# Kernel optimization log

Hardware: AMD Instinct MI355X
Metric: run time of the kernel (lower is better)

## Reference

```python
import jax, jax.numpy as jnp
import numpy as np
import math

NHEADS = 4


def _mab(Q, K, qw, qb, kw, kb, vw, vb, ow, ob, mask):
    """MAB2 from tripletformer: multi-head attention (head split via cat(split,0)),
    softmax scale uses sqrt(FULL dim_V), masked_fill(mask==0, -1e10), residual on
    the projected Q, then O + relu(fc_o(O))."""
    dv = qw.shape[1]
    dh = dv // NHEADS
    B, Nq, _ = Q.shape
    Nk = K.shape[1]
    Qh = (Q @ qw + qb).reshape(B, Nq, NHEADS, dh).transpose(0, 2, 1, 3)  # B,h,Nq,dh
    Kh = (K @ kw + kb).reshape(B, Nk, NHEADS, dh).transpose(0, 2, 1, 3)
    Vh = (K @ vw + vb).reshape(B, Nk, NHEADS, dh).transpose(0, 2, 1, 3)
    att = jnp.einsum('bhqd,bhkd->bhqk', Qh, Kh) * (1.0 / math.sqrt(dv))
    att = jnp.where(mask, att, jnp.asarray(-1e10, att.dtype))
    A = jax.nn.softmax(att, axis=-1)
    Oh = Qh + jnp.einsum('bhqk,bhkd->bhqd', A, Vh)
    O = Oh.transpose(0, 2, 1, 3).reshape(B, Nq, dv)
    return O + jax.nn.relu(O @ ow + ob)


def _forward(context_x, value, mask, obs_len, iff_w, iff_b, ind_points,
             q0w, q0b, k0w, k0b, v0w, v0b, o0w, o0b,
             q1w, q1b, k1w, k1b, v1w, v1b, o1w, o1b):
    B, L = context_x.shape
    D = value.shape[-1]
    mflat = mask.reshape(B, L * D)
    # stable stream compaction: observed entries first, original (time-major,
    # channel-minor) order preserved; truncate to static obs_len
    order = jnp.argsort(-mflat, axis=-1, stable=True)[:, :obs_len]  # (B, N)
    T = jnp.broadcast_to(context_x[:, :, None], (B, L, D)).reshape(B, L * D)
    C = jnp.broadcast_to(jnp.arange(D, dtype=jnp.int32), (B, L, D)).reshape(B, L * D)
    U = value.reshape(B, L * D)
    take = lambda a: jnp.take_along_axis(a, order, axis=-1)
    T_, U_, mk_ = take(T), take(U), take(mflat)
    Ch = jax.nn.one_hot(take(C), D, dtype=value.dtype)  # one_hot(num_classes=dim-2)
    X = jnp.concatenate([Ch, T_[..., None], U_[..., None]], axis=-1) * mk_[..., None]
    Y = jax.nn.relu(X @ iff_w + iff_b) * mk_[..., None]
    key_valid = mk_ > 0                        # (B, N)
    mask1 = key_valid[:, None, None, :]        # mab0: mask padded keys
    mask2 = key_valid[:, None, :, None]        # mab1: mask padded query rows
    Z = Y
    n_layers = ind_points.shape[0]
    for i in range(n_layers):
        I = jnp.broadcast_to(ind_points[i], (B,) + ind_points[i].shape)
        H = _mab(I, Z, q0w[i], q0b[i], k0w[i], k0b[i], v0w[i], v0b[i], o0w[i], o0b[i], mask1)
        Zn = _mab(Z, H, q1w[i], q1b[i], k1w[i], k1b[i], v1w[i], v1b[i], o1w[i], o1b[i], mask2)
        Z = Zn * mk_[..., None] + Z
    return Z, mk_[..., None]


def setup_inputs() -> dict:
    B, L, D, OBS, DK, M, NL = 16, 512, 41, 4096, 128, 128, 3
    key = jax.random.key(0)
    ks = jax.random.split(key, 16)
    context_x = jnp.sort(jax.random.uniform(ks[0], (B, L), dtype=jnp.float32), axis=-1)
    value = jax.random.normal(ks[1], (B, L, D), dtype=jnp.float32)
    # exactly OBS observed entries per batch row -> static packed length
    r = jax.random.uniform(ks[2], (B, L * D))
    kth = jnp.sort(r, axis=-1)[:, OBS]
    mask = (r < kth[:, None]).astype(jnp.float32).reshape(B, L, D)

    def w(k, shape, fan):
        return jax.random.normal(k, shape, dtype=jnp.float32) / math.sqrt(fan)

    inp = dict(
        context_x=context_x, value=value, mask=mask, obs_len=OBS,
        iff_w=w(ks[3], (D + 2, DK), D + 2), iff_b=jnp.zeros((DK,), jnp.float32),
        ind_points=w(ks[4], (NL, M, DK), DK),
    )
    for j, n in enumerate(['q0', 'k0', 'v0', 'o0', 'q1', 'k1', 'v1', 'o1']):
        inp[n + 'w'] = w(ks[5 + j], (NL, DK, DK), DK)
        inp[n + 'b'] = jnp.zeros((NL, DK), jnp.float32)
    return inp


def reference(context_x, value, mask, obs_len, iff_w, iff_b, ind_points,
              q0w, q0b, k0w, k0b, v0w, v0b, o0w, o0b,
              q1w, q1b, k1w, k1b, v1w, v1b, o1w, o1b):
    return _forward(context_x, value, mask, obs_len, iff_w, iff_b, ind_points,
                    q0w, q0b, k0w, k0b, v0w, v0b, o0w, o0b,
                    q1w, q1b, k1w, k1b, v1w, v1b, o1w, o1b)
```

## Files before the change

kernel.cpp:

```cpp
#include <hip/hip_runtime.h>
#include <math.h>

#define NBATCH 16
#define SEQL   512
#define DIM    41
#define LDFLAT (SEQL*DIM)
#define OBS    4096
#define DK     128
#define NH     4
#define DH     32

typedef short bf16x8 __attribute__((ext_vector_type(8)));
typedef short short8v __attribute__((ext_vector_type(8)));
typedef float floatx4 __attribute__((ext_vector_type(4)));

__device__ __forceinline__ short f2bf(float f) {
  union { float f; unsigned u; } v;
  v.f = f;
  unsigned r = (v.u + 0x7fffu + ((v.u >> 16) & 1u)) >> 16;
  return (short)r;
}
__device__ __forceinline__ float bf2f(short s) {
  union { unsigned u; float f; } v;
  v.u = ((unsigned)(unsigned short)s) << 16;
// ... 18 lines not shown
#pragma unroll
  for (int k = 0; k < 4; k++) {
    int i = tid * 8 + k * 2048;
    *(int4*)&Wl[swz(i >> 7, i & 127)] = s.v[k];
  }
}
typedef struct { int4 v[2]; } WStageF;
__device__ __forceinline__ void stage_load_f(WStageF& s,
                                             const short* __restrict__ W,
                                             int tid) {
#pragma unroll
  for (int k = 0; k < 2; k++)
    s.v[k] = *(const int4*)&W[(size_t)tid * 8 + (size_t)k * 8192];
}
__device__ __forceinline__ void stage_write_f(short* Wl, const WStageF& s,
                                              int tid) {
#pragma unroll
  for (int k = 0; k < 2; k++) {
    int i = tid * 8 + k * 8192;
    *(int4*)&Wl[swz(i >> 7, i & 127)] = s.v[k];
  }
}

__device__ __forceinline__ void gemm4_s(const short* Wl, const bf16x8 af[4],
                                        int lm, int quad, floatx4 acc[4]) {
#pragma unroll
  for (int nt = 0; nt < 4; nt++) acc[nt] = (floatx4){0.f, 0.f, 0.f, 0.f};
#pragma unroll
  for (int kc = 0; kc < 4; kc++) {
    bf16x8 a = af[kc];
#pragma unroll
    for (int nt = 0; nt < 4; nt++) {
      bf16x8 b = *(const bf16x8*)&Wl[swz(nt * 16 + lm, kc * 32 + quad * 8)];
      acc[nt] = __builtin_amdgcn_mfma_f32_16x16x32_bf16(a, b, acc[nt], 0, 0, 0);
    }
  }
}
__device__ __forceinline__ void gemm2_s(const short* Wl, const bf16x8 af[4],
                                        int colq, int lm, int quad,
                                        floatx4 acc[2]) {
#pragma unroll
  for (int nt = 0; nt < 2; nt++) acc[nt] = (floatx4){0.f, 0.f, 0.f, 0.f};
#pragma unroll
  for (int kc = 0; kc < 4; kc++) {
    bf16x8 a = af[kc];
#pragma unroll
    for (int nt = 0; nt < 2; nt++) {
      bf16x8 b = *(const bf16x8*)&Wl[swz(colq * 32 + nt * 16 + lm,
                                         kc * 32 + quad * 8)];
      acc[nt] = __builtin_amdgcn_mfma_f32_16x16x32_bf16(a, b, acc[nt], 0, 0, 0);
    }
  }
}
__device__ __forceinline__ void load_af_s(const short* Xl, int strip, int lm,
                                          int quad, bf16x8 af[4]) {
#pragma unroll
  for (int kc = 0; kc < 4; kc++)
    af[kc] = *(const bf16x8*)&Xl[swz(strip * 16 + lm, kc * 32 + quad * 8)];
}
__device__ __forceinline__ void store_sl4(short* Sl, const floatx4 acc[4],
                                          const float* __restrict__ bias,
                                          int wv, int lm, int quad,
                                          int colbase) {
#pragma unroll
  for (int nt = 0; nt < 4; nt++) {
    int col = colbase + nt * 16 + lm;
    float bn = bias[col];
#pragma unroll
    for (int r = 0; r < 4; r++)
      Sl[swz(wv * 16 + quad * 4 + r, col)] = f2bf(acc[nt][r] + bn);
  }
}
__device__ __forceinline__ void write_hs_s(const short* Sl,
                                           short* __restrict__ out, int rb,
                                           int nshift, int tid) {
  int rr = tid >> 2, hh = tid & 3;
  int r = rb + rr;
  int bb = r >> nshift, nn = r & ((1 << nshift) - 1);
  size_t o = (((size_t)(bb * NH + hh) << nshift) + nn) * 32;
#pragma unroll
  for (int j = 0; j < 4; j++)
    *(int4*)&out[o + j * 8] = *(int4*)&Sl[swz(rr, hh * 32 + j * 8)];
}
__device__ __forceinline__ void write_hs_q(const short* Sl,
                                           short* __restrict__ out, int rb,
                                           int nshift, int strip, int colq,
                                           int lane) {
  int rr = strip * 16 + (lane >> 2);
  int r = rb + rr;
  int bb = r >> nshift, nn = r & ((1 << nshift) - 1);
  size_t o = (((size_t)(bb * NH + colq) << nshift) + nn) * 32 + (lane & 3) * 8;
  *(int4*)&out[o] = *(const int4*)&Sl[swz(rr, colq * 32 + (lane & 3) * 8)];
}

__global__ __launch_bounds__(1024) void prep_build_kernel(
    const float* __restrict__ q0w, const float* __restrict__ k0w,
    const float* __restrict__ v0w, const float* __restrict__ o0w,
    const float* __restrict__ q1w, const float* __restrict__ k1w,
    const float* __restrict__ v1w, const float* __restrict__ o1w,
    short* __restrict__ Wt,
    const float* __restrict__ mask, int* __restrict__ order,
    float* __restrict__ mk_out, float* __restrict__ mk_out2) {
  __shared__ float Tl[128 * 132];
  __shared__ int wsums[16];
  __shared__ int s_total_ones;
  __shared__ int s_chunk_ones;
  __shared__ int s_ones_base;
  __shared__ int s_zeros_base;
  int tid = threadIdx.x;

  if (blockIdx.x < 24) {
    int id = blockIdx.x, l = id >> 3, wi = id & 7;
    const float* s;
    switch (wi) {
      case 0: s = q0w; break; case 1: s = k0w; break;
      case 2: s = v0w; break; case 3: s = o0w; break;
      case 4: s = q1w; break; case 5: s = k1w; break;
      case 6: s = v1w; break; default: s = o1w; break;
    }
    s += (size_t)l * 16384;
    for (int i = tid * 4; i < 16384; i += 4096) {
      int k = i >> 7, n = i & 127;
      float4 x = *(const float4*)&s[i];
      Tl[k * 132 + n + 0] = x.x; Tl[k * 132 + n + 1] = x.y;
      Tl[k * 132 + n + 2] = x.z; Tl[k * 132 + n + 3] = x.w;
    }
    __syncthreads();
    short* dst = Wt + (size_t)id * 16384;
    int n = tid >> 3, k0 = (tid & 7) * 16;
    for (int jc = 0; jc < 2; jc++) {
      short8v t;
#pragma unroll
      for (int j = 0; j < 8; j++) t[j] = f2bf(Tl[(k0 + jc * 8 + j) * 132 + n]);
      *(short8v*)&dst[n * 128 + k0 + jc * 8] = t;
    }
// ... 8 lines not shown
  for (int j = tid; j < LDFLAT; j += 1024) cnt += (m[j] > 0.f) ? 1 : 0;
  for (int off = 32; off > 0; off >>= 1) cnt += __shfl_xor(cnt, off);
  if (lane == 0) wsums[w] = cnt;
  __syncthreads();
  if (tid == 0) {
    int t = 0;
    for (int i = 0; i < 16; i++) t += wsums[i];
    s_total_ones = t; s_ones_base = 0; s_zeros_base = 0;
  }
  __syncthreads();
  int total_ones = s_total_ones;

  for (int c0 = 0; c0 < LDFLAT; c0 += 1024) {
    __syncthreads();
    int j = c0 + tid;
    bool valid = (j < LDFLAT);
    float mv = valid ? m[j] : 0.f;
    int one = (valid && mv > 0.f) ? 1 : 0;
    int v = one;
    for (int off = 1; off < 64; off <<= 1) {
      int t = __shfl_up(v, (unsigned)off);
      if (lane >= off) v += t;
    }
    if (lane == 63) wsums[w] = v;
    __syncthreads();
    if (tid == 0) {
      int run = 0;
      for (int i = 0; i < 16; i++) { int t = wsums[i]; wsums[i] = run; run += t; }
      s_chunk_ones = run;
    }
    __syncthreads();
    int ones_before = (v - one) + wsums[w];
    int ob = s_ones_base, zb = s_zeros_base, chunk_ones = s_chunk_ones;
    int rem = LDFLAT - c0;
    int chunk_valid = rem < 1024 ? rem : 1024;
    int valid_before = tid < rem ? tid : rem;
    if (valid) {
      int pos = one ? (ob + ones_before)
                    : (total_ones + zb + (valid_before - ones_before));
      if (pos < OBS) {
        order[b * OBS + pos] = j;
        mk_out[b * OBS + pos] = mv;
        mk_out2[b * OBS + pos] = mv;
      }
    }
    __syncthreads();
    if (tid == 0) {
      s_ones_base = ob + chunk_ones;
      s_zeros_base = zb + (chunk_valid - chunk_ones);
    }
  }
}

__global__ __launch_bounds__(256, 3) void fusedA_kernel(
    const int* __restrict__ order, const float* __restrict__ mk_g,
    const float* __restrict__ cx, const float* __restrict__ value,
    const float* __restrict__ iff_w, const float* __restrict__ iff_b,
    float* __restrict__ Z,
    const short* __restrict__ Wk, const float* __restrict__ kbias,
    short* __restrict__ Kb,
    const short* __restrict__ Wv, const float* __restrict__ vbias,
    short* __restrict__ Vb,
    const short* __restrict__ Wq, const float* __restrict__ qbias,
    short* __restrict__ Qb,
    const float* __restrict__ indp, const short* __restrict__ WtAll,
    const float* __restrict__ q0b_all, short* __restrict__ qh_b) {
  __shared__ __align__(16) short Xl[64 * 128];
  __shared__ __align__(16) short WlA[64 * 128];
  __shared__ __align__(16) short WlB[64 * 128];
  int tid = threadIdx.x;
  int wv = tid >> 6, lane = tid & 63, lm = lane & 15, quad = lane >> 4;
  int r_l = lane >> 2, seg = lane & 3;
  int lrow = wv * 16 + r_l;

  if (blockIdx.x >= 1024) {
    int id = blockIdx.x - 1024;
    int l = id >> 1, rbq = (id & 1) * 64;
    const float* X = indp + (size_t)l * 16384 + (size_t)rbq * 128;
    const short* W = WtAll + (size_t)(l * 8) * 16384;
    const float* bias = q0b_all + (size_t)l * 128;
    short* out = qh_b + (size_t)l * 16384;
    WStageH sA, sB;
    stage_load_h(sA, W, tid);
    stage_load_h(sB, W + 8192, tid);
    const float* Xr = X + (size_t)lrow * 128;
#pragma unroll
    for (int jj = 0; jj < 8; jj++) {
      int col = seg * 32 + jj * 4;
      float4 x = *(const float4*)&Xr[col];
      *(short4*)&Xl[swz(lrow, col)] =
          make_short4(f2bf(x.x), f2bf(x.y), f2bf(x.z), f2bf(x.w));
    }
    stage_write_h(WlA, sA, tid);
    stage_write_h(WlB, sB, tid);
    __syncthreads();
    bf16x8 af[4];
    load_af_s(Xl, wv, lm, quad, af);
    floatx4 acc[4];
    gemm4_s(WlA, af, lm, quad, acc);
    store_sl4(Xl, acc, bias, wv, lm, quad, 0);
    gemm4_s(WlB, af, lm, quad, acc);
    store_sl4(Xl, acc, bias, wv, lm, quad, 64);
    write_hs_s(Xl, out, rbq, 7, tid);
    return;
  }

  int rb = blockIdx.x * 64;
  WStageH s0; stage_load_h(s0, Wk, tid);
  int grow = rb + lrow;
  int bb = grow >> 12;
  int j = order[grow];
  int l = j / DIM, d = j - l * DIM;
  float t = cx[bb * SEQL + l];
  float u = value[(size_t)bb * LDFLAT + j];
  float mkv = mk_g[grow];
#pragma unroll
  for (int jj = 0; jj < 8; jj++) {
    int col = seg * 32 + jj * 4;
    float4 w0 = *(const float4*)&iff_w[d * DK + col];
    float4 w1 = *(const float4*)&iff_w[41 * DK + col];
    float4 w2 = *(const float4*)&iff_w[42 * DK + col];
    float4 b4 = *(const float4*)&iff_b[col];
    float4 z;
    z.x = fmaxf(w0.x + t * w1.x + u * w2.x + b4.x, 0.f) * mkv;
    z.y = fmaxf(w0.y + t * w1.y + u * w2.y + b4.y, 0.f) * mkv;
    z.z = fmaxf(w0.z + t * w1.z + u * w2.z + b4.z, 0.f) * mkv;
    z.w = fmaxf(w0.w + t * w1.w + u * w2.w + b4.w, 0.f) * mkv;
    *(float4*)&Z[(size_t)grow * DK + col] = z;
    *(short4*)&Xl[swz(lrow, col)] =
        make_short4(f2bf(z.x), f2bf(z.y), f2bf(z.z), f2bf(z.w));
  }
  stage_write_h(WlA, s0, tid);
  __syncthreads();
  WStageH s1; stage_load_h(s1, Wk + 8192, tid);
  bf16x8 af[4];
  load_af_s(Xl, wv, lm, quad, af);
  floatx4 acc[4];
  gemm4_s(WlA, af, lm, quad, acc);
  store_sl4(Xl, acc, kbias, wv, lm, quad, 0);
  stage_write_h(WlB, s1, tid);
  __syncthreads();
  WStageH s2; stage_load_h(s2, Wv, tid);
  gemm4_s(WlB, af, lm, quad, acc);
  store_sl4(Xl, acc, kbias, wv, lm, quad, 64);
  write_hs_s(Xl, Kb, rb, 12, tid);
  stage_write_h(WlA, s2, tid);
  __syncthreads();
  WStageH s3; stage_load_h(s3, Wv + 8192, tid);
  gemm4_s(WlA, af, lm, quad, acc);
  store_sl4(Xl, acc, vbias, wv, lm, quad, 0);
  stage_write_h(WlB, s3, tid);
  __syncthreads();
  WStageH s4; stage_load_h(s4, Wq, tid);
  gemm4_s(WlB, af, lm, quad, acc);
  store_sl4(Xl, acc, vbias, wv, lm, quad, 64);
  write_hs_s(Xl, Vb, rb, 12, tid);
  stage_write_h(WlA, s4, tid);
  __syncthreads();
  WStageH s5; stage_load_h(s5, Wq + 8192, tid);
  gemm4_s(WlA, af, lm, quad, acc);
  store_sl4(Xl, acc, qbias, wv, lm, quad, 0);
  stage_write_h(WlB, s5, tid);
  __syncthreads();
  gemm4_s(WlB, af, lm, quad, acc);
  store_sl4(Xl, acc, qbias, wv, lm, quad, 64);
  write_hs_s(Xl, Qb, rb, 12, tid);
}

__global__ __launch_bounds__(256) void attn1_kernel(
    const short* __restrict__ Qh,
    const short* __restrict__ Kh, const short* __restrict__ Vh,
    const float* __restrict__ mk,
    float* __restrict__ Opart, float* __restrict__ mpart,
    float* __restrict__ lpart) {
  __shared__ __align__(16) short Ql[128 * 40];
  __shared__ __align__(16) short Kc[64 * 40];
  __shared__ __align__(16) short Vtc[32 * 72];
  __shared__ __align__(16) short Pl[128 * 72];
  __shared__ float mkc[64];
  int bh = blockIdx.x;
  int b = bh >> 2, h = bh & 3;
  int ks = blockIdx.y;
  int tid = threadIdx.x;
  int wv = tid >> 6, lane = tid & 63, lm = lane & 15, quad = lane >> 4;

  const short* qbg = Qh + (size_t)h * 128 * 32;
  for (int i = tid * 8; i < 128 * 32; i += 2048) {
    int r = i >> 5, c = i & 31;
    *(int4*)&Ql[r * 40 + c] = *(const int4*)&qbg[i];
  }
  __syncthreads();
  bf16x8 aq[2];
  aq[0] = *(bf16x8*)&Ql[(wv * 32 + lm) * 40 + quad * 8];
  aq[1] = *(bf16x8*)&Ql[(wv * 32 + 16 + lm) * 40 + quad * 8];

  float m_i[2][4], l_i[2][4];
  floatx4 oacc[2][2];
#pragma unroll
  for (int mt = 0; mt < 2; mt++) {
#pragma unroll
    for (int r = 0; r < 4; r++) { m_i[mt][r] = -1e30f; l_i[mt][r] = 0.f; }
    oacc[mt][0] = (floatx4){0.f, 0.f, 0.f, 0.f};
    oacc[mt][1] = (floatx4){0.f, 0.f, 0.f, 0.f};
  }
  const float scale = 0.08838834764831845f;
  const short* kbase = Kh + ((size_t)bh * OBS + ks * 512) * 32;
  const short* vbase = Vh + ((size_t)bh * OBS + ks * 512) * 32;
  const float* mkb = mk + (size_t)b * OBS + ks * 512;

  for (int ch = 0; ch < 8; ch++) {
    __syncthreads();
    {
      int i = tid * 8;
      int r = i >> 5, c = i & 31;
      *(int4*)&Kc[r * 40 + c] = *(const int4*)&kbase[ch * 2048 + i];
      int4 vv4 = *(const int4*)&vbase[ch * 2048 + i];
      short* vv = (short*)&vv4;
#pragma unroll
      for (int j = 0; j < 8; j++) Vtc[(c + j) * 72 + r] = vv[j];
// ... 132 lines not shown
    o4.z = f2bf(bf2f(qs[2]) + oa2 * li);
    o4.w = f2bf(bf2f(qs[3]) + oa3 * li);
    *(short4*)&Xl[swz(rr, hh * 32 + c4)] = o4;
  }
  stage_write_f(WlA, sWo, tid);
  __syncthreads();
  bf16x8 afO[4];
  load_af_s(Xl, strip, lm, quad, afO);
  __syncthreads();
  WStageF sWk; stage_load_f(sWk, Wk, tid);
  floatx4 acc[2];
  gemm2_s(WlA, afO, colq, lm, quad, acc);
#pragma unroll
  for (int nt = 0; nt < 2; nt++) {
    int col = colq * 32 + nt * 16 + lm;
    float bn = obias[col];
#pragma unroll
    for (int r = 0; r < 4; r++) {
      int row = strip * 16 + quad * 4 + r;
      float ov = bf2f(Xl[swz(row, col)]);
      Xl[swz(row, col)] = f2bf(ov + fmaxf(acc[nt][r] + bn, 0.f));
    }
  }
  stage_write_f(WlB, sWk, tid);
  __syncthreads();
  bf16x8 afH[4];
  load_af_s(Xl, strip, lm, quad, afH);
  __syncthreads();
  WStageF sWv; stage_load_f(sWv, Wv, tid);
  gemm2_s(WlB, afH, colq, lm, quad, acc);
#pragma unroll
  for (int nt = 0; nt < 2; nt++) {
    int col = colq * 32 + nt * 16 + lm;
    float bn = kbias[col];
#pragma unroll
    for (int r = 0; r < 4; r++)
      Xl[swz(strip * 16 + quad * 4 + r, col)] = f2bf(acc[nt][r] + bn);
  }
  write_hs_q(Xl, khb, rb, 7, strip, colq, lane);
  stage_write_f(WlA, sWv, tid);
  __syncthreads();
  gemm2_s(WlA, afH, colq, lm, quad, acc);
#pragma unroll
  for (int nt = 0; nt < 2; nt++) {
    int col = colq * 32 + nt * 16 + lm;
    float bn = vbias[col];
#pragma unroll
    for (int r = 0; r < 4; r++)
      Xl[swz(strip * 16 + quad * 4 + r, col)] = f2bf(acc[nt][r] + bn);
  }
  write_hs_q(Xl, vhb, rb, 7, strip, colq, lane);
}

__global__ __launch_bounds__(256) void attn2_kernel(
    const short* __restrict__ Qh, const short* __restrict__ Kh,
    const short* __restrict__ Vh, short* __restrict__ O) {
  __shared__ __align__(16) short Kl[128 * 40];
  __shared__ __align__(16) short Vt[32 * 136];
  __shared__ __align__(16) short Ql[64 * 40];
  __shared__ __align__(16) short Pl[64 * 136];
  int bh = blockIdx.x;
  int b = bh >> 2, h = bh & 3;
  int q0 = blockIdx.y * 64;
  int tid = threadIdx.x;
  int wv = tid >> 6, lane = tid & 63, lm = lane & 15, quad = lane >> 4;
  const short* kb = Kh + (size_t)bh * 128 * 32;
  const short* vb = Vh + (size_t)bh * 128 * 32;
  const short* qb = Qh + ((size_t)bh * OBS + q0) * 32;

  for (int i = tid * 8; i < 128 * 32; i += 2048) {
    int r = i >> 5, c = i & 31;
    *(int4*)&Kl[r * 40 + c] = *(const int4*)&kb[i];
  }
  for (int i = tid * 8; i < 64 * 32; i += 2048) {
    int r = i >> 5, c = i & 31;
    *(int4*)&Ql[r * 40 + c] = *(const int4*)&qb[i];
  }
  for (int i = tid * 8; i < 128 * 32; i += 2048) {
    int r = i >> 5, c = i & 31;
    int4 vv4 = *(const int4*)&vb[i];
    short* vv = (short*)&vv4;
#pragma unroll
    for (int j = 0; j < 8; j++) Vt[(c + j) * 136 + r] = vv[j];
  }
  __syncthreads();

  const float scale = 0.08838834764831845f;
  bf16x8 afrag = *(bf16x8*)&Ql[(wv * 16 + lm) * 40 + quad * 8];
  floatx4 sf[8];
#pragma unroll
  for (int nt = 0; nt < 8; nt++) {
    bf16x8 bfrag = *(bf16x8*)&Kl[(nt * 16 + lm) * 40 + quad * 8];
    floatx4 z = {0.f, 0.f, 0.f, 0.f};
    sf[nt] = __builtin_amdgcn_mfma_f32_16x16x32_bf16(afrag, bfrag, z, 0, 0, 0);
  }
#pragma unroll
  for (int nt = 0; nt < 8; nt++) sf[nt] *= scale;
  float linv[4];
#pragma unroll
  for (int r = 0; r < 4; r++) {
    float mx = sf[0][r];
#pragma unroll
    for (int nt = 1; nt < 8; nt++) mx = fmaxf(mx, sf[nt][r]);
    mx = fmaxf(mx, __shfl_xor(mx, 1));
    mx = fmaxf(mx, __shfl_xor(mx, 2));
    mx = fmaxf(mx, __shfl_xor(mx, 4));
    mx = fmaxf(mx, __shfl_xor(mx, 8));
    float sum = 0.f;
#pragma unroll
    for (int nt = 0; nt < 8; nt++) {
      float p = __expf(sf[nt][r] - mx);
      sf[nt][r] = p;
      sum += p;
    }
    sum += __shfl_xor(sum, 1);
    sum += __shfl_xor(sum, 2);
    sum += __shfl_xor(sum, 4);
    sum += __shfl_xor(sum, 8);
    linv[r] = 1.f / sum;
  }
#pragma unroll
  for (int nt = 0; nt < 8; nt++)
#pragma unroll
    for (int r = 0; r < 4; r++)
      Pl[(wv * 16 + quad * 4 + r) * 136 + nt * 16 + lm] = f2bf(sf[nt][r]);

  floatx4 oacc[2] = {{0.f, 0.f, 0.f, 0.f}, {0.f, 0.f, 0.f, 0.f}};
#pragma unroll
  for (int kc = 0; kc < 4; kc++) {
    bf16x8 pf = *(bf16x8*)&Pl[(wv * 16 + lm) * 136 + kc * 32 + quad * 8];
#pragma unroll
    for (int nt2 = 0; nt2 < 2; nt2++) {
      bf16x8 vf = *(bf16x8*)&Vt[(nt2 * 16 + lm) * 136 + kc * 32 + quad * 8];
      oacc[nt2] = __builtin_amdgcn_mfma_f32_16x16x32_bf16(pf, vf, oacc[nt2], 0, 0, 0);
    }
  }
  short* Ol = Pl;
#pragma unroll
  for (int nt2 = 0; nt2 < 2; nt2++) {
#pragma unroll
    for (int r = 0; r < 4; r++) {
      int qrow = wv * 16 + quad * 4 + r;
      float q = bf2f(Ql[qrow * 40 + nt2 * 16 + lm]);
      Ol[qrow * 136 + nt2 * 16 + lm] = f2bf(q + oacc[nt2][r] * linv[r]);
    }
  }
  int rr = tid >> 2, seg = tid & 3;
  size_t o = ((size_t)b * OBS + q0 + rr) * 128 + h * 32 + seg * 8;
  *(int4*)&O[o] = *(int4*)&Ol[rr * 136 + seg * 8];
}

__global__ __launch_bounds__(256, 3) void fusedC_kernel(
    const short* __restrict__ Ob, const short* __restrict__ Wo,
    const float* __restrict__ obias, const float* __restrict__ mk,
    const float* __restrict__ Zin, float* __restrict__ Zout,
    const short* __restrict__ Wk, const float* __restrict__ kbias,
    short* __restrict__ Kb,
    const short* __restrict__ Wv, const float* __restrict__ vbias,
    short* __restrict__ Vb,
    const short* __restrict__ Wq, const float* __restrict__ qbias,
    short* __restrict__ Qb) {
  __shared__ __align__(16) short Xl[64 * 128];
  __shared__ __align__(16) short WlA[64 * 128];
  __shared__ __align__(16) short WlB[64 * 128];
  int tid = threadIdx.x;
  int rb = blockIdx.x * 64;
  int wv = tid >> 6, lane = tid & 63, lm = lane & 15, quad = lane >> 4;

  WStageH s0; stage_load_h(s0, Wo, tid);
  bf16x8 afO[4];
  {
    const short* arow = Ob + (size_t)(rb + wv * 16 + lm) * 128;
#pragma unroll
    for (int kc = 0; kc < 4; kc++) {
      afO[kc] = *(const bf16x8*)&arow[kc * 32 + quad * 8];
      *(bf16x8*)&Xl[swz(wv * 16 + lm, kc * 32 + quad * 8)] = afO[kc];
    }
  }
  int row0 = wv * 16 + quad * 4;
  float mkv[4];
#pragma unroll
  for (int r = 0; r < 4; r++) mkv[r] = mk[rb + row0 + r];
  stage_write_h(WlA, s0, tid);
  __syncthreads();
  WStageH s1; stage_load_h(s1, Wo + 8192, tid);
  floatx4 acc[4];
  gemm4_s(WlA, afO, lm, quad, acc);
#pragma unroll
  for (int nt = 0; nt < 4; nt++) {
    int col = nt * 16 + lm;
    float bn = obias[col];
#pragma unroll
    for (int r = 0; r < 4; r++) {
      int row = row0 + r;
      size_t g = (size_t)(rb + row) * 128 + col;
      float ov = bf2f(Xl[swz(row, col)]);
      float f = ov + fmaxf(acc[nt][r] + bn, 0.f);
      float zv = Zin[g] + f * mkv[r];
      Zout[g] = zv;
      Xl[swz(row, col)] = f2bf(zv);
    }
  }
  stage_write_h(WlB, s1, tid);
  __syncthreads();
  WStageH s2;
  if (Wk) stage_load_h(s2, Wk, tid);
  gemm4_s(WlB, afO, lm, quad, acc);
#pragma unroll
  for (int nt = 0; nt < 4; nt++) {
    int col = 64 + nt * 16 + lm;
    float bn = obias[col];
#pragma unroll
    for (int r = 0; r < 4; r++) {
      int row = row0 + r;
      size_t g = (size_t)(rb + row) * 128 + col;
      float ov = bf2f(Xl[swz(row, col)]);
      float f = ov + fmaxf(acc[nt][r] + bn, 0.f);
      float zv = Zin[g] + f * mkv[r];
      Zout[g] = zv;
      Xl[swz(row, col)] = f2bf(zv);
    }
  }
  if (Wk == nullptr) return;
  bf16x8 af[4];
  load_af_s(Xl, wv, lm, quad, af);
  stage_write_h(WlA, s2, tid);
  __syncthreads();
  WStageH s3; stage_load_h(s3, Wk + 8192, tid);
  gemm4_s(WlA, af, lm, quad, acc);
  store_sl4(Xl, acc, kbias, wv, lm, quad, 0);
  stage_write_h(WlB, s3, tid);
  __syncthreads();
  WStageH s4; stage_load_h(s4, Wv, tid);
  gemm4_s(WlB, af, lm, quad, acc);
  store_sl4(Xl, acc, kbias, wv, lm, quad, 64);
  write_hs_s(Xl, Kb, rb, 12, tid);
  stage_write_h(WlA, s4, tid);
  __syncthreads();
  WStageH s5; stage_load_h(s5, Wv + 8192, tid);
  gemm4_s(WlA, af, lm, quad, acc);
  store_sl4(Xl, acc, vbias, wv, lm, quad, 0);
  stage_write_h(WlB, s5, tid);
  __syncthreads();
  WStageH s6; stage_load_h(s6, Wq, tid);
  gemm4_s(WlB, af, lm, quad, acc);
  store_sl4(Xl, acc, vbias, wv, lm, quad, 64);
  write_hs_s(Xl, Vb, rb, 12, tid);
  stage_write_h(WlA, s6, tid);
  __syncthreads();
  WStageH s7; stage_load_h(s7, Wq + 8192, tid);
  gemm4_s(WlA, af, lm, quad, acc);
  store_sl4(Xl, acc, qbias, wv, lm, quad, 0);
  stage_write_h(WlB, s7, tid);
  __syncthreads();
  gemm4_s(WlB, af, lm, quad, acc);
  store_sl4(Xl, acc, qbias, wv, lm, quad, 64);
  write_hs_s(Xl, Qb, rb, 12, tid);
}

extern "C" void kernel_launch(void* const* d_in, const int* in_sizes, int n_in,
                              void* d_out, int out_size, void* d_ws,
                              size_t ws_size, hipStream_t stream) {
  const float* cx    = (const float*)d_in[0];
  const float* value = (const float*)d_in[1];
  const float* mask  = (const float*)d_in[2];
  const float* iff_w = (const float*)d_in[4];
  const float* iff_b = (const float*)d_in[5];
  const float* indp  = (const float*)d_in[6];
  const float* q0w = (const float*)d_in[7];  const float* q0b = (const float*)d_in[8];
  const float* k0w = (const float*)d_in[9];  const float* k0b = (const float*)d_in[10];
  const float* v0w = (const float*)d_in[11]; const float* v0b = (const float*)d_in[12];
  const float* o0w = (const float*)d_in[13]; const float* o0b = (const float*)d_in[14];
  const float* q1w = (const float*)d_in[15]; const float* q1b = (const float*)d_in[16];
  const float* k1w = (const float*)d_in[17]; const float* k1b = (const float*)d_in[18];
  const float* v1w = (const float*)d_in[19]; const float* v1b = (const float*)d_in[20];
  const float* o1w = (const float*)d_in[21]; const float* o1b = (const float*)d_in[22];

  char* ws = (char*)d_ws;
  short* Wt    = (short*)ws;  ws += (size_t)24 * 16384 * 2;
  int*   order = (int*)ws;    ws += (size_t)NBATCH * OBS * 4;
  float* mk_g  = (float*)ws;  ws += (size_t)NBATCH * OBS * 4;
  float* Z     = (float*)ws;  ws += (size_t)NBATCH * OBS * DK * 4;
  short* Qb    = (short*)ws;  ws += (size_t)NBATCH * OBS * DK * 2;
  short* Kb    = (short*)ws;  ws += (size_t)NBATCH * OBS * DK * 2;
  short* Vb    = (short*)ws;  ws += (size_t)NBATCH * OBS * DK * 2;
  short* Ob    = (short*)ws;  ws += (size_t)NBATCH * OBS * DK * 2;
  short* qh_b  = (short*)ws;  ws += (size_t)3 * 128 * DK * 2;
  short* khb   = (short*)ws;  ws += (size_t)NBATCH * NH * 128 * DH * 2;
  short* vhb   = (short*)ws;  ws += (size_t)NBATCH * NH * 128 * DH * 2;
  float* Opart = (float*)ws;  ws += (size_t)8 * 64 * 128 * 32 * 4;
  float* mpart = (float*)ws;  ws += (size_t)8 * 64 * 128 * 4;
  float* lpart = (float*)ws;  ws += (size_t)8 * 64 * 128 * 4;

  float* outZ  = (float*)d_out;
  float* outMk = outZ + (size_t)NBATCH * OBS * DK;

  prep_build_kernel<<<40, 1024, 0, stream>>>(q0w, k0w, v0w, o0w, q1w, k1w,
                                             v1w, o1w, Wt, mask, order, mk_g,
                                             outMk);

  const short* W[3][8];
  for (int l = 0; l < 3; l++)
    for (int wi = 0; wi < 8; wi++) W[l][wi] = Wt + (size_t)(l * 8 + wi) * 16384;

  fusedA_kernel<<<1030, 256, 0, stream>>>(
      order, mk_g, cx, value, iff_w, iff_b, Z,
      W[0][1], k0b, Kb, W[0][2], v0b, Vb, W[0][4], q1b, Qb,
      indp, Wt, q0b, qh_b);

  for (int l = 0; l < 3; l++) {
    attn1_kernel<<<dim3(64, 8), 256, 0, stream>>>(
        qh_b + (size_t)l * 16384, Kb, Vb, mk_g, Opart, mpart, lpart);
    fusedB_kernel<<<32, 1024, 0, stream>>>(
        Opart, mpart, lpart, qh_b + (size_t)l * 16384,
        W[l][3], o0b + (size_t)l * 128,
        W[l][5], k1b + (size_t)l * 128,
        W[l][6], v1b + (size_t)l * 128, khb, vhb);
    attn2_kernel<<<dim3(64, 64), 256, 0, stream>>>(Qb, khb, vhb, Ob);
    if (l < 2) {
      fusedC_kernel<<<1024, 256, 0, stream>>>(
          Ob, W[l][7], o1b + (size_t)l * 128, mk_g, Z, Z,
          W[l + 1][1], k0b + (size_t)(l + 1) * 128, Kb,
          W[l + 1][2], v0b + (size_t)(l + 1) * 128, Vb,
          W[l + 1][4], q1b + (size_t)(l + 1) * 128, Qb);
    } else {
      fusedC_kernel<<<1024, 256, 0, stream>>>(
          Ob, W[l][7], o1b + (size_t)l * 128, mk_g, Z, outZ,
          nullptr, nullptr, nullptr, nullptr, nullptr, nullptr,
          nullptr, nullptr, nullptr);
    }
  }
}
```

Before: 461.6 us.

## Double row tile per block in fusedA, fusedC and attn2 to amortize weight staging

Each block of fusedA, fusedC and attn2 now covers 128 rows instead of 64. Each wave handles two 16-row strips against the same staged weight or K/V tiles, and the grids are halved. The aim is to halve how often each weight slice is staged through LDS and to cut per-block overhead and barriers. In exchange it doubles the activation LDS footprint and register pressure, lowers the occupancy hint from 3 to 2, and leaves fewer blocks to fill the GPU.

```diff
diff --git a/kernel.cpp b/kernel.cpp
--- a/kernel.cpp
+++ b/kernel.cpp
@@ -94,15 +94,15 @@
     }
   }
 }
-__device__ __forceinline__ void load_af_s(const short* Xl, int strip, int lm,
+__device__ __forceinline__ void load_af_s(const short* Xl, int sb, int lm,
                                           int quad, bf16x8 af[4]) {
 #pragma unroll
   for (int kc = 0; kc < 4; kc++)
-    af[kc] = *(const bf16x8*)&Xl[swz(strip * 16 + lm, kc * 32 + quad * 8)];
+    af[kc] = *(const bf16x8*)&Xl[swz(sb * 16 + lm, kc * 32 + quad * 8)];
 }
 __device__ __forceinline__ void store_sl4(short* Sl, const floatx4 acc[4],
                                           const float* __restrict__ bias,
-                                          int wv, int lm, int quad,
+                                          int sb, int lm, int quad,
                                           int colbase) {
 #pragma unroll
   for (int nt = 0; nt < 4; nt++) {
@@ -110,19 +110,24 @@
     float bn = bias[col];
 #pragma unroll
     for (int r = 0; r < 4; r++)
-      Sl[swz(wv * 16 + quad * 4 + r, col)] = f2bf(acc[nt][r] + bn);
-  }
-}
-__device__ __forceinline__ void write_hs_s(const short* Sl,
-                                           short* __restrict__ out, int rb,
-                                           int nshift, int tid) {
-  int rr = tid >> 2, hh = tid & 3;
-  int r = rb + rr;
-  int bb = r >> nshift, nn = r & ((1 << nshift) - 1);
-  size_t o = (((size_t)(bb * NH + hh) << nshift) + nn) * 32;
-#pragma unroll
-  for (int j = 0; j < 4; j++)
-    *(int4*)&out[o + j * 8] = *(int4*)&Sl[swz(rr, hh * 32 + j * 8)];
+      Sl[swz(sb * 16 + quad * 4 + r, col)] = f2bf(acc[nt][r] + bn);
+  }
+}
+__device__ __forceinline__ void write_hs2(const short* Sl,
+                                          short* __restrict__ out, int rb,
+                                          int nshift, int wv, int lane) {
+#pragma unroll
+  for (int p = 0; p < 2; p++) {
+    int pair = p * 64 + lane;
+    int rr = wv * 32 + (pair >> 2);
+    int hh = pair & 3;
+    int r = rb + rr;
+    int bb = r >> nshift, nn = r & ((1 << nshift) - 1);
+    size_t o = (((size_t)(bb * NH + hh) << nshift) + nn) * 32;
+#pragma unroll
+    for (int j = 0; j < 4; j++)
+      *(int4*)&out[o + j * 8] = *(const int4*)&Sl[swz(rr, hh * 32 + j * 8)];
+  }
 }
 __device__ __forceinline__ void write_hs_q(const short* Sl,
                                            short* __restrict__ out, int rb,
@@ -237,7 +242,7 @@
   }
 }
 
-__global__ __launch_bounds__(256, 3) void fusedA_kernel(
+__global__ __launch_bounds__(256, 2) void fusedA_kernel(
     const int* __restrict__ order, const float* __restrict__ mk_g,
     const float* __restrict__ cx, const float* __restrict__ value,
     const float* __restrict__ iff_w, const float* __restrict__ iff_b,
@@ -250,18 +255,17 @@
     short* __restrict__ Qb,
     const float* __restrict__ indp, const short* __restrict__ WtAll,
     const float* __restrict__ q0b_all, short* __restrict__ qh_b) {
-  __shared__ __align__(16) short Xl[64 * 128];
+  __shared__ __align__(16) short Xl[128 * 128];
   __shared__ __align__(16) short WlA[64 * 128];
   __shared__ __align__(16) short WlB[64 * 128];
   int tid = threadIdx.x;
   int wv = tid >> 6, lane = tid & 63, lm = lane & 15, quad = lane >> 4;
-  int r_l = lane >> 2, seg = lane & 3;
-  int lrow = wv * 16 + r_l;
-
-  if (blockIdx.x >= 1024) {
-    int id = blockIdx.x - 1024;
-    int l = id >> 1, rbq = (id & 1) * 64;
-    const float* X = indp + (size_t)l * 16384 + (size_t)rbq * 128;
+  int r_l = lane >> 1, seg = lane & 1;
+  int lrow = wv * 32 + r_l;
+
+  if (blockIdx.x >= 512) {
+    int l = blockIdx.x - 512;
+    const float* X = indp + (size_t)l * 16384;
     const short* W = WtAll + (size_t)(l * 8) * 16384;
     const float* bias = q0b_all + (size_t)l * 128;
     short* out = qh_b + (size_t)l * 16384;
@@ -270,8 +274,8 @@
     stage_load_h(sB, W + 8192, tid);
     const float* Xr = X + (size_t)lrow * 128;
 #pragma unroll
-    for (int jj = 0; jj < 8; jj++) {
-      int col = seg * 32 + jj * 4;
+    for (int jj = 0; jj < 16; jj++) {
+      int col = seg * 64 + jj * 4;
       float4 x = *(const float4*)&Xr[col];
       *(short4*)&Xl[swz(lrow, col)] =
           make_short4(f2bf(x.x), f2bf(x.y), f2bf(x.z), f2bf(x.w));
@@ -279,18 +283,23 @@
     stage_write_h(WlA, sA, tid);
     stage_write_h(WlB, sB, tid);
     __syncthreads();
-    bf16x8 af[4];
-    load_af_s(Xl, wv, lm, quad, af);
+    bf16x8 af[2][4];
+    load_af_s(Xl, 2 * wv, lm, quad, af[0]);
+    load_af_s(Xl, 2 * wv + 1, lm, quad, af[1]);
     floatx4 acc[4];
-    gemm4_s(WlA, af, lm, quad, acc);
-    store_sl4(Xl, acc, bias, wv, lm, quad, 0);
-    gemm4_s(WlB, af, lm, quad, acc);
-    store_sl4(Xl, acc, bias, wv, lm, quad, 64);
-    write_hs_s(Xl, out, rbq, 7, tid);
+    gemm4_s(WlA, af[0], lm, quad, acc);
+    store_sl4(Xl, acc, bias, 2 * wv, lm, quad, 0);
+    gemm4_s(WlA, af[1], lm, quad, acc);
+    store_sl4(Xl, acc, bias, 2 * wv + 1, lm, quad, 0);
+    gemm4_s(WlB, af[0], lm, quad, acc);
+    store_sl4(Xl, acc, bias, 2 * wv, lm, quad, 64);
+    gemm4_s(WlB, af[1], lm, quad, acc);
+    store_sl4(Xl, acc, bias, 2 * wv + 1, lm, quad, 64);
+    write_hs2(Xl, out, 0, 7, wv, lane);
     return;
   }
 
-  int rb = blockIdx.x * 64;
+  int rb = blockIdx.x * 128;
   WStageH s0; stage_load_h(s0, Wk, tid);
   int grow = rb + lrow;
   int bb = grow >> 12;
@@ -300,8 +309,8 @@
   float u = value[(size_t)bb * LDFLAT + j];
   float mkv = mk_g[grow];
 #pragma unroll
-  for (int jj = 0; jj < 8; jj++) {
-    int col = seg * 32 + jj * 4;
+  for (int jj = 0; jj < 16; jj++) {
+    int col = seg * 64 + jj * 4;
     float4 w0 = *(const float4*)&iff_w[d * DK + col];
     float4 w1 = *(const float4*)&iff_w[41 * DK + col];
     float4 w2 = *(const float4*)&iff_w[42 * DK + col];
@@ -318,38 +327,51 @@
   stage_write_h(WlA, s0, tid);
   __syncthreads();
   WStageH s1; stage_load_h(s1, Wk + 8192, tid);
-  bf16x8 af[4];
-  load_af_s(Xl, wv, lm, quad, af);
+  bf16x8 af[2][4];
+  load_af_s(Xl, 2 * wv, lm, quad, af[0]);
+  load_af_s(Xl, 2 * wv + 1, lm, quad, af[1]);
   floatx4 acc[4];
-  gemm4_s(WlA, af, lm, quad, acc);
-  store_sl4(Xl, acc, kbias, wv, lm, quad, 0);
+  gemm4_s(WlA, af[0], lm, quad, acc);
+  store_sl4(Xl, acc, kbias, 2 * wv, lm, quad, 0);
+  gemm4_s(WlA, af[1], lm, quad, acc);
+  store_sl4(Xl, acc, kbias, 2 * wv + 1, lm, quad, 0);
   stage_write_h(WlB, s1, tid);
   __syncthreads();
   WStageH s2; stage_load_h(s2, Wv, tid);
-  gemm4_s(WlB, af, lm, quad, acc);
-  store_sl4(Xl, acc, kbias, wv, lm, quad, 64);
-  write_hs_s(Xl, Kb, rb, 12, tid);
+  gemm4_s(WlB, af[0], lm, quad, acc);
+  store_sl4(Xl, acc, kbias, 2 * wv, lm, quad, 64);
+  gemm4_s(WlB, af[1], lm, quad, acc);
+  store_sl4(Xl, acc, kbias, 2 * wv + 1, lm, quad, 64);
+  write_hs2(Xl, Kb, rb, 12, wv, lane);
   stage_write_h(WlA, s2, tid);
   __syncthreads();
   WStageH s3; stage_load_h(s3, Wv + 8192, tid);
-  gemm4_s(WlA, af, lm, quad, acc);
-  store_sl4(Xl, acc, vbias, wv, lm, quad, 0);
+  gemm4_s(WlA, af[0], lm, quad, acc);
+  store_sl4(Xl, acc, vbias, 2 * wv, lm, quad, 0);
+  gemm4_s(WlA, af[1], lm, quad, acc);
+  store_sl4(Xl, acc, vbias, 2 * wv + 1, lm, quad, 0);
   stage_write_h(WlB, s3, tid);
   __syncthreads();
   WStageH s4; stage_load_h(s4, Wq, tid);
-  gemm4_s(WlB, af, lm, quad, acc);
-  store_sl4(Xl, acc, vbias, wv, lm, quad, 64);
-  write_hs_s(Xl, Vb, rb, 12, tid);
+  gemm4_s(WlB, af[0], lm, quad, acc);
+  store_sl4(Xl, acc, vbias, 2 * wv, lm, quad, 64);
+  gemm4_s(WlB, af[1], lm, quad, acc);
+  store_sl4(Xl, acc, vbias, 2 * wv + 1, lm, quad, 64);
+  write_hs2(Xl, Vb, rb, 12, wv, lane);
   stage_write_h(WlA, s4, tid);
   __syncthreads();
   WStageH s5; stage_load_h(s5, Wq + 8192, tid);
-  gemm4_s(WlA, af, lm, quad, acc);
-  store_sl4(Xl, acc, qbias, wv, lm, quad, 0);
+  gemm4_s(WlA, af[0], lm, quad, acc);
+  store_sl4(Xl, acc, qbias, 2 * wv, lm, quad, 0);
+  gemm4_s(WlA, af[1], lm, quad, acc);
+  store_sl4(Xl, acc, qbias, 2 * wv + 1, lm, quad, 0);
   stage_write_h(WlB, s5, tid);
   __syncthreads();
-  gemm4_s(WlB, af, lm, quad, acc);
-  store_sl4(Xl, acc, qbias, wv, lm, quad, 64);
-  write_hs_s(Xl, Qb, rb, 12, tid);
+  gemm4_s(WlB, af[0], lm, quad, acc);
+  store_sl4(Xl, acc, qbias, 2 * wv, lm, quad, 64);
+  gemm4_s(WlB, af[1], lm, quad, acc);
+  store_sl4(Xl, acc, qbias, 2 * wv + 1, lm, quad, 64);
+  write_hs2(Xl, Qb, rb, 12, wv, lane);
 }
 
 __global__ __launch_bounds__(256) void attn1_kernel(
@@ -588,16 +610,16 @@
   write_hs_q(Xl, vhb, rb, 7, strip, colq, lane);
 }
 
-__global__ __launch_bounds__(256) void attn2_kernel(
+__global__ __launch_bounds__(256, 2) void attn2_kernel(
     const short* __restrict__ Qh, const short* __restrict__ Kh,
     const short* __restrict__ Vh, short* __restrict__ O) {
   __shared__ __align__(16) short Kl[128 * 40];
   __shared__ __align__(16) short Vt[32 * 136];
-  __shared__ __align__(16) short Ql[64 * 40];
-  __shared__ __align__(16) short Pl[64 * 136];
+  __shared__ __align__(16) short Ql[128 * 40];
+  __shared__ __align__(16) short Pl[128 * 136];
   int bh = blockIdx.x;
   int b = bh >> 2, h = bh & 3;
-  int q0 = blockIdx.y * 64;
+  int q0 = blockIdx.y * 128;
   int tid = threadIdx.x;
   int wv = tid >> 6, lane = tid & 63, lm = lane & 15, quad = lane >> 4;
   const short* kb = Kh + (size_t)bh * 128 * 32;
@@ -608,7 +630,7 @@
     int r = i >> 5, c = i & 31;
     *(int4*)&Kl[r * 40 + c] = *(const int4*)&kb[i];
   }
-  for (int i = tid * 8; i < 64 * 32; i += 2048) {
+  for (int i = tid * 8; i < 128 * 32; i += 2048) {
     int r = i >> 5, c = i & 31;
     *(int4*)&Ql[r * 40 + c] = *(const int4*)&qb[i];
   }
@@ -622,71 +644,90 @@
   __syncthreads();
 
   const float scale = 0.08838834764831845f;
-  bf16x8 afrag = *(bf16x8*)&Ql[(wv * 16 + lm) * 40 + quad * 8];
-  floatx4 sf[8];
+  bf16x8 aq[2];
+  aq[0] = *(bf16x8*)&Ql[(wv * 32 + lm) * 40 + quad * 8];
+  aq[1] = *(bf16x8*)&Ql[(wv * 32 + 16 + lm) * 40 + quad * 8];
+  floatx4 sf[2][8];
 #pragma unroll
   for (int nt = 0; nt < 8; nt++) {
     bf16x8 bfrag = *(bf16x8*)&Kl[(nt * 16 + lm) * 40 + quad * 8];
     floatx4 z = {0.f, 0.f, 0.f, 0.f};
-    sf[nt] = __builtin_amdgcn_mfma_f32_16x16x32_bf16(afrag, bfrag, z, 0, 0, 0);
-  }
-#pragma unroll
-  for (int nt = 0; nt < 8; nt++) sf[nt] *= scale;
-  float linv[4];
-#pragma unroll
-  for (int r = 0; r < 4; r++) {
-    float mx = sf[0][r];
-#pragma unroll
-    for (int nt = 1; nt < 8; nt++) mx = fmaxf(mx, sf[nt][r]);
-    mx = fmaxf(mx, __shfl_xor(mx, 1));
-    mx = fmaxf(mx, __shfl_xor(mx, 2));
-    mx = fmaxf(mx, __shfl_xor(mx, 4));
-    mx = fmaxf(mx, __shfl_xor(mx, 8));
-    float sum = 0.f;
-#pragma unroll
-    for (int nt = 0; nt < 8; nt++) {
-      float p = __expf(sf[nt][r] - mx);
-      sf[nt][r] = p;
-      sum += p;
-    }
-    sum += __shfl_xor(sum, 1);
-    sum += __shfl_xor(sum, 2);
-    sum += __shfl_xor(sum, 4);
-    sum += __shfl_xor(sum, 8);
-    linv[r] = 1.f / sum;
-  }
-#pragma unroll
-  for (int nt = 0; nt < 8; nt++)
-#pragma unroll
-    for (int r = 0; r < 4; r++)
-      Pl[(wv * 16 + quad * 4 + r) * 136 + nt * 16 + lm] = f2bf(sf[nt][r]);
-
-  floatx4 oacc[2] = {{0.f, 0.f, 0.f, 0.f}, {0.f, 0.f, 0.f, 0.f}};
+    sf[0][nt] = __builtin_amdgcn_mfma_f32_16x16x32_bf16(aq[0], bfrag, z, 0, 0, 0);
+    sf[1][nt] = __builtin_amdgcn_mfma_f32_16x16x32_bf16(aq[1], bfrag, z, 0, 0, 0);
+  }
+  float linv[2][4];
+#pragma unroll
+  for (int s = 0; s < 2; s++) {
+#pragma unroll
+    for (int nt = 0; nt < 8; nt++) sf[s][nt] *= scale;
+#pragma unroll
+    for (int r = 0; r < 4; r++) {
+      float mx = sf[s][0][r];
+#pragma unroll
+      for (int nt = 1; nt < 8; nt++) mx = fmaxf(mx, sf[s][nt][r]);
+      mx = fmaxf(mx, __shfl_xor(mx, 1));
+      mx = fmaxf(mx, __shfl_xor(mx, 2));
+      mx = fmaxf(mx, __shfl_xor(mx, 4));
+      mx = fmaxf(mx, __shfl_xor(mx, 8));
+      float sum = 0.f;
+#pragma unroll
+      for (int nt = 0; nt < 8; nt++) {
+        float p = __expf(sf[s][nt][r] - mx);
+        sf[s][nt][r] = p;
+        sum += p;
+      }
+      sum += __shfl_xor(sum, 1);
+      sum += __shfl_xor(sum, 2);
+      sum += __shfl_xor(sum, 4);
+      sum += __shfl_xor(sum, 8);
+      linv[s][r] = 1.f / sum;
+    }
+#pragma unroll
+    for (int nt = 0; nt < 8; nt++)
+#pragma unroll
+      for (int r = 0; r < 4; r++)
+        Pl[(wv * 32 + s * 16 + quad * 4 + r) * 136 + nt * 16 + lm] =
+            f2bf(sf[s][nt][r]);
+  }
+
+  floatx4 oacc[2][2];
+#pragma unroll
+  for (int s = 0; s < 2; s++) {
+    oacc[s][0] = (floatx4){0.f, 0.f, 0.f, 0.f};
+    oacc[s][1] = (floatx4){0.f, 0.f, 0.f, 0.f};
+  }
 #pragma unroll
   for (int kc = 0; kc < 4; kc++) {
-    bf16x8 pf = *(bf16x8*)&Pl[(wv * 16 + lm) * 136 + kc * 32 + quad * 8];
-#pragma unroll
-    for (int nt2 = 0; nt2 < 2; nt2++) {
-      bf16x8 vf = *(bf16x8*)&Vt[(nt2 * 16 + lm) * 136 + kc * 32 + quad * 8];
-      oacc[nt2] = __builtin_amdgcn_mfma_f32_16x16x32_bf16(pf, vf, oacc[nt2], 0, 0, 0);
+    bf16x8 vf0 = *(bf16x8*)&Vt[lm * 136 + kc * 32 + quad * 8];
+    bf16x8 vf1 = *(bf16x8*)&Vt[(16 + lm) * 136 + kc * 32 + quad * 8];
+#pragma unroll
+    for (int s = 0; s < 2; s++) {
+      bf16x8 pf = *(bf16x8*)&Pl[(wv * 32 + s * 16 + lm) * 136 + kc * 32 + quad * 8];
+      oacc[s][0] = __builtin_amdgcn_mfma_f32_16x16x32_bf16(pf, vf0, oacc[s][0], 0, 0, 0);
+      oacc[s][1] = __builtin_amdgcn_mfma_f32_16x16x32_bf16(pf, vf1, oacc[s][1], 0, 0, 0);
     }
   }
   short* Ol = Pl;
 #pragma unroll
-  for (int nt2 = 0; nt2 < 2; nt2++) {
-#pragma unroll
-    for (int r = 0; r < 4; r++) {
-      int qrow = wv * 16 + quad * 4 + r;
-      float q = bf2f(Ql[qrow * 40 + nt2 * 16 + lm]);
-      Ol[qrow * 136 + nt2 * 16 + lm] = f2bf(q + oacc[nt2][r] * linv[r]);
-    }
-  }
-  int rr = tid >> 2, seg = tid & 3;
-  size_t o = ((size_t)b * OBS + q0 + rr) * 128 + h * 32 + seg * 8;
-  *(int4*)&O[o] = *(int4*)&Ol[rr * 136 + seg * 8];
-}
-
-__global__ __launch_bounds__(256, 3) void fusedC_kernel(
+  for (int s = 0; s < 2; s++)
+#pragma unroll
+    for (int nt2 = 0; nt2 < 2; nt2++)
+#pragma unroll
+      for (int r = 0; r < 4; r++) {
+        int qrow = wv * 32 + s * 16 + quad * 4 + r;
+        float q = bf2f(Ql[qrow * 40 + nt2 * 16 + lm]);
+        Ol[qrow * 136 + nt2 * 16 + lm] = f2bf(q + oacc[s][nt2][r] * linv[s][r]);
+      }
+#pragma unroll
+  for (int p = 0; p < 2; p++) {
+    int pair = p * 64 + lane;
+    int rr = wv * 32 + (pair >> 2), sg = pair & 3;
+    size_t o = ((size_t)b * OBS + q0 + rr) * 128 + h * 32 + sg * 8;
+    *(int4*)&O[o] = *(int4*)&Ol[rr * 136 + sg * 8];
+  }
+}
+
+__global__ __launch_bounds__(256, 2) void fusedC_kernel(
     const short* __restrict__ Ob, const short* __restrict__ Wo,
     const float* __restrict__ obias, const float* __restrict__ mk,
     const float* __restrict__ Zin, float* __restrict__ Zout,
@@ -696,102 +737,126 @@
     short* __restrict__ Vb,
     const short* __restrict__ Wq, const float* __restrict__ qbias,
     short* __restrict__ Qb) {
-  __shared__ __align__(16) short Xl[64 * 128];
+  __shared__ __align__(16) short Xl[128 * 128];
   __shared__ __align__(16) short WlA[64 * 128];
   __shared__ __align__(16) short WlB[64 * 128];
   int tid = threadIdx.x;
-  int rb = blockIdx.x * 64;
+  int rb = blockIdx.x * 128;
   int wv = tid >> 6, lane = tid & 63, lm = lane & 15, quad = lane >> 4;
 
   WStageH s0; stage_load_h(s0, Wo, tid);
-  bf16x8 afO[4];
-  {
-    const short* arow = Ob + (size_t)(rb + wv * 16 + lm) * 128;
+  bf16x8 afO[2][4];
+#pragma unroll
+  for (int s = 0; s < 2; s++) {
+    const short* arow = Ob + (size_t)(rb + wv * 32 + s * 16 + lm) * 128;
 #pragma unroll
     for (int kc = 0; kc < 4; kc++) {
-      afO[kc] = *(const bf16x8*)&arow[kc * 32 + quad * 8];
-      *(bf16x8*)&Xl[swz(wv * 16 + lm, kc * 32 + quad * 8)] = afO[kc];
-    }
-  }
-  int row0 = wv * 16 + quad * 4;
-  float mkv[4];
-#pragma unroll
-  for (int r = 0; r < 4; r++) mkv[r] = mk[rb + row0 + r];
+      afO[s][kc] = *(const bf16x8*)&arow[kc * 32 + quad * 8];
+      *(bf16x8*)&Xl[swz(wv * 32 + s * 16 + lm, kc * 32 + quad * 8)] = afO[s][kc];
+    }
+  }
+  float mkv[2][4];
+#pragma unroll
+  for (int s = 0; s < 2; s++)
+#pragma unroll
+    for (int r = 0; r < 4; r++)
+      mkv[s][r] = mk[rb + wv * 32 + s * 16 + quad * 4 + r];
   stage_write_h(WlA, s0, tid);
   __syncthreads();
   WStageH s1; stage_load_h(s1, Wo + 8192, tid);
   floatx4 acc[4];
-  gemm4_s(WlA, afO, lm, quad, acc);
-#pragma unroll
-  for (int nt = 0; nt < 4; nt++) {
-    int col = nt * 16 + lm;
-    float bn = obias[col];
-#pragma unroll
-    for (int r = 0; r < 4; r++) {
-      int row = row0 + r;
-      size_t g = (size_t)(rb + row) * 128 + col;
-      float ov = bf2f(Xl[swz(row, col)]);
-      float f = ov + fmaxf(acc[nt][r] + bn, 0.f);
-      float zv = Zin[g] + f * mkv[r];
-      Zout[g] = zv;
-      Xl[swz(row, col)] = f2bf(zv);
+#pragma unroll
+  for (int s = 0; s < 2; s++) {
+    gemm4_s(WlA, afO[s], lm, quad, acc);
+    int row0 = wv * 32 + s * 16 + quad * 4;
+#pragma unroll
+    for (int nt = 0; nt < 4; nt++) {
+      int col = nt * 16 + lm;
+      float bn = obias[col];
+#pragma unroll
+      for (int r = 0; r < 4; r++) {
+        int row = row0 + r;
+        size_t g = (size_t)(rb + row) * 128 + col;
+        float ov = bf2f(Xl[swz(row, col)]);
+        float f = ov + fmaxf(acc[nt][r] + bn, 0.f);
+        float zv = Zin[g] + f * mkv[s][r];
+        Zout[g] = zv;
+        Xl[swz(row, col)] = f2bf(zv);
+      }
     }
   }
   stage_write_h(WlB, s1, tid);
   __syncthreads();
   WStageH s2;
   if (Wk) stage_load_h(s2, Wk, tid);
-  gemm4_s(WlB, afO, lm, quad, acc);
-#pragma unroll
-  for (int nt = 0; nt < 4; nt++) {
-    int col = 64 + nt * 16 + lm;
-    float bn = obias[col];
-#pragma unroll
-    for (int r = 0; r < 4; r++) {
-      int row = row0 + r;
-      size_t g = (size_t)(rb + row) * 128 + col;
-      float ov = bf2f(Xl[swz(row, col)]);
-      float f = ov + fmaxf(acc[nt][r] + bn, 0.f);
-      float zv = Zin[g] + f * mkv[r];
-      Zout[g] = zv;
-      Xl[swz(row, col)] = f2bf(zv);
+#pragma unroll
+  for (int s = 0; s < 2; s++) {
+    gemm4_s(WlB, afO[s], lm, quad, acc);
+    int row0 = wv * 32 + s * 16 + quad * 4;
+#pragma unroll
+    for (int nt = 0; nt < 4; nt++) {
+      int col = 64 + nt * 16 + lm;
+      float bn = obias[col];
+#pragma unroll
+      for (int r = 0; r < 4; r++) {
+        int row = row0 + r;
+        size_t g = (size_t)(rb + row) * 128 + col;
+        float ov = bf2f(Xl[swz(row, col)]);
+        float f = ov + fmaxf(acc[nt][r] + bn, 0.f);
+        float zv = Zin[g] + f * mkv[s][r];
+        Zout[g] = zv;
+        Xl[swz(row, col)] = f2bf(zv);
+      }
     }
   }
   if (Wk == nullptr) return;
-  bf16x8 af[4];
-  load_af_s(Xl, wv, lm, quad, af);
+  bf16x8 af[2][4];
+  load_af_s(Xl, 2 * wv, lm, quad, af[0]);
+  load_af_s(Xl, 2 * wv + 1, lm, quad, af[1]);
   stage_write_h(WlA, s2, tid);
   __syncthreads();
   WStageH s3; stage_load_h(s3, Wk + 8192, tid);
-  gemm4_s(WlA, af, lm, quad, acc);
-  store_sl4(Xl, acc, kbias, wv, lm, quad, 0);
+  gemm4_s(WlA, af[0], lm, quad, acc);
+  store_sl4(Xl, acc, kbias, 2 * wv, lm, quad, 0);
+  gemm4_s(WlA, af[1], lm, quad, acc);
+  store_sl4(Xl, acc, kbias, 2 * wv + 1, lm, quad, 0);
   stage_write_h(WlB, s3, tid);
   __syncthreads();
   WStageH s4; stage_load_h(s4, Wv, tid);
-  gemm4_s(WlB, af, lm, quad, acc);
-  store_sl4(Xl, acc, kbias, wv, lm, quad, 64);
-  write_hs_s(Xl, Kb, rb, 12, tid);
+  gemm4_s(WlB, af[0], lm, quad, acc);
+  store_sl4(Xl, acc, kbias, 2 * wv, lm, quad, 64);
+  gemm4_s(WlB, af[1], lm, quad, acc);
+  store_sl4(Xl, acc, kbias, 2 * wv + 1, lm, quad, 64);
+  write_hs2(Xl, Kb, rb, 12, wv, lane);
   stage_write_h(WlA, s4, tid);
   __syncthreads();
   WStageH s5; stage_load_h(s5, Wv + 8192, tid);
-  gemm4_s(WlA, af, lm, quad, acc);
-  store_sl4(Xl, acc, vbias, wv, lm, quad, 0);
+  gemm4_s(WlA, af[0], lm, quad, acc);
+  store_sl4(Xl, acc, vbias, 2 * wv, lm, quad, 0);
+  gemm4_s(WlA, af[1], lm, quad, acc);
+  store_sl4(Xl, acc, vbias, 2 * wv + 1, lm, quad, 0);
   stage_write_h(WlB, s5, tid);
   __syncthreads();
   WStageH s6; stage_load_h(s6, Wq, tid);
-  gemm4_s(WlB, af, lm, quad, acc);
-  store_sl4(Xl, acc, vbias, wv, lm, quad, 64);
-  write_hs_s(Xl, Vb, rb, 12, tid);
+  gemm4_s(WlB, af[0], lm, quad, acc);
+  store_sl4(Xl, acc, vbias, 2 * wv, lm, quad, 64);
+  gemm4_s(WlB, af[1], lm, quad, acc);
+  store_sl4(Xl, acc, vbias, 2 * wv + 1, lm, quad, 64);
+  write_hs2(Xl, Vb, rb, 12, wv, lane);
   stage_write_h(WlA, s6, tid);
   __syncthreads();
   WStageH s7; stage_load_h(s7, Wq + 8192, tid);
-  gemm4_s(WlA, af, lm, quad, acc);
-  store_sl4(Xl, acc, qbias, wv, lm, quad, 0);
+  gemm4_s(WlA, af[0], lm, quad, acc);
+  store_sl4(Xl, acc, qbias, 2 * wv, lm, quad, 0);
+  gemm4_s(WlA, af[1], lm, quad, acc);
+  store_sl4(Xl, acc, qbias, 2 * wv + 1, lm, quad, 0);
   stage_write_h(WlB, s7, tid);
   __syncthreads();
-  gemm4_s(WlB, af, lm, quad, acc);
-  store_sl4(Xl, acc, qbias, wv, lm, quad, 64);
-  write_hs_s(Xl, Qb, rb, 12, tid);
+  gemm4_s(WlB, af[0], lm, quad, acc);
+  store_sl4(Xl, acc, qbias, 2 * wv, lm, quad, 64);
+  gemm4_s(WlB, af[1], lm, quad, acc);
+  store_sl4(Xl, acc, qbias, 2 * wv + 1, lm, quad, 64);
+  write_hs2(Xl, Qb, rb, 12, wv, lane);
 }
 
 extern "C" void kernel_launch(void* const* d_in, const int* in_sizes, int n_in,
@@ -839,7 +904,7 @@
   for (int l = 0; l < 3; l++)
     for (int wi = 0; wi < 8; wi++) W[l][wi] = Wt + (size_t)(l * 8 + wi) * 16384;
 
-  fusedA_kernel<<<1030, 256, 0, stream>>>(
+  fusedA_kernel<<<515, 256, 0, stream>>>(
       order, mk_g, cx, value, iff_w, iff_b, Z,
       W[0][1], k0b, Kb, W[0][2], v0b, Vb, W[0][4], q1b, Qb,
       indp, Wt, q0b, qh_b);
@@ -852,15 +917,15 @@
         W[l][3], o0b + (size_t)l * 128,
         W[l][5], k1b + (size_t)l * 128,
         W[l][6], v1b + (size_t)l * 128, khb, vhb);
-    attn2_kernel<<<dim3(64, 64), 256, 0, stream>>>(Qb, khb, vhb, Ob);
+    attn2_kernel<<<dim3(64, 32), 256, 0, stream>>>(Qb, khb, vhb, Ob);
     if (l < 2) {
-      fusedC_kernel<<<1024, 256, 0, stream>>>(
+      fusedC_kernel<<<512, 256, 0, stream>>>(
           Ob, W[l][7], o1b + (size_t)l * 128, mk_g, Z, Z,
           W[l + 1][1], k0b + (size_t)(l + 1) * 128, Kb,
           W[l + 1][2], v0b + (size_t)(l + 1) * 128, Vb,
           W[l + 1][4], q1b + (size_t)(l + 1) * 128, Qb);
     } else {
-      fusedC_kernel<<<1024, 256, 0, stream>>>(
+      fusedC_kernel<<<512, 256, 0, stream>>>(
           Ob, W[l][7], o1b + (size_t)l * 128, mk_g, Z, outZ,
           nullptr, nullptr, nullptr, nullptr, nullptr, nullptr,
           nullptr, nullptr, nullptr);
```

New measurement: 480.9 us. +4.2%, slower.
